# Optimization experiments

Measured on AMD Instinct MI355X. Metric: run time of the kernel, lower is better.

Reference implementation:

```python
import math
import jax, jax.numpy as jnp
import numpy as np

EMB = 1024
NHEADS = 16
CTX = 2048
LN_EPS = 1e-5


def new_gelu(x):
    c = math.sqrt(2.0 / math.pi)
    return 0.5 * x * (1.0 + jnp.tanh(c * (x + 0.044715 * x * x * x)))


def layer_norm(x, g, b):
    mu = jnp.mean(x, axis=-1, keepdims=True)
    var = jnp.mean(jnp.square(x - mu), axis=-1, keepdims=True)
    return (x - mu) * jax.lax.rsqrt(var + LN_EPS) * g + b


def setup_inputs() -> dict:
    key = jax.random.key(0)
    ks = jax.random.split(key, 12)
    s = 0.02
    return {
        "x": jax.random.normal(ks[0], (2, 2048, EMB), dtype=jnp.float32),
        "ln1_g": jnp.ones((EMB,), jnp.float32),
        "ln1_b": jnp.zeros((EMB,), jnp.float32),
        "W_attn": jax.random.normal(ks[1], (EMB, 3 * EMB), jnp.float32) * s,
        "b_attn": jnp.zeros((3 * EMB,), jnp.float32),
        "W_attn_proj": jax.random.normal(ks[2], (EMB, EMB), jnp.float32) * s,
        "b_attn_proj": jnp.zeros((EMB,), jnp.float32),
        "ln2_g": jnp.ones((EMB,), jnp.float32),
        "ln2_b": jnp.zeros((EMB,), jnp.float32),
        "W_fc": jax.random.normal(ks[3], (EMB, 4 * EMB), jnp.float32) * s,
        "b_fc": jnp.zeros((4 * EMB,), jnp.float32),
        "W_mlp_proj": jax.random.normal(ks[4], (4 * EMB, EMB), jnp.float32) * s,
        "b_mlp_proj": jnp.zeros((EMB,), jnp.float32),
    }


def reference(x, ln1_g, ln1_b, W_attn, b_attn, W_attn_proj, b_attn_proj,
              ln2_g, ln2_b, W_fc, b_fc, W_mlp_proj, b_mlp_proj):
    B, S, E = x.shape
    hd = E // NHEADS

    # x = ln_1(x)
    x = layer_norm(x, ln1_g, ln1_b)

    # attention on normalized x
    qkv = x @ W_attn + b_attn                      # [B,S,3E]
    q, k, v = jnp.split(qkv, 3, axis=-1)
    q = q.reshape(B, S, NHEADS, hd).transpose(0, 2, 1, 3)  # [B,H,S,hd]
    k = k.reshape(B, S, NHEADS, hd).transpose(0, 2, 1, 3)
    v = v.reshape(B, S, NHEADS, hd).transpose(0, 2, 1, 3)

    attn = jnp.einsum("bhqd,bhkd->bhqk", q, k) * (1.0 / math.sqrt(hd))
    causal = jnp.tril(jnp.ones((S, S), dtype=bool))
    attn = jnp.where(causal[None, None], attn, -jnp.inf)
    attn = jax.nn.softmax(attn, axis=-1)
    out = jnp.einsum("bhqk,bhkd->bhqd", attn, v)   # [B,H,S,hd]
    out = out.transpose(0, 2, 1, 3).reshape(B, S, E)
    out = out @ W_attn_proj + b_attn_proj

    x = x + out

    # x = ln_2(x)
    x = layer_norm(x, ln2_g, ln2_b)

    # MLP on normalized x
    h = new_gelu(x @ W_fc + b_fc)
    h = h @ W_mlp_proj + b_mlp_proj
    return x + h
```

## Files before the change

kernel.cpp:

```cpp
#include <hip/hip_runtime.h>
#include <cstdint>

typedef __attribute__((ext_vector_type(8))) short bf16x8;
typedef __attribute__((ext_vector_type(4))) float f32x4;
typedef __attribute__((ext_vector_type(4))) unsigned short u16x4;
typedef unsigned short u16;

#define LOG2E 1.44269504088896340736f

__device__ __forceinline__ u16 f2bf(float f) {
  unsigned u = __builtin_bit_cast(unsigned, f);
  u += 0x7FFFu + ((u >> 16) & 1u);
  return (u16)(u >> 16);
}
__device__ __forceinline__ float bf2f(u16 h) {
  return __builtin_bit_cast(float, ((unsigned)h) << 16);
}

#define GLOAD_LDS16(g, l)                                                              \
  __builtin_amdgcn_global_load_lds((const __attribute__((address_space(1))) void*)(g), \
                                   (__attribute__((address_space(3))) void*)(l), 16, 0, 0)

__global__ __launch_bounds__(256) void k_transpose_bf16(
    const float* __restrict__ W, u16* __restrict__ Wt, int K, int N) {
  __shared__ float tile[32][33];
  const int tid = threadIdx.x;
  const int tx = tid & 31, ty = tid >> 5;
  const int n0 = blockIdx.x * 32, k0 = blockIdx.y * 32;
#pragma unroll
  for (int i = 0; i < 32; i += 8)
    tile[ty + i][tx] = W[(size_t)(k0 + ty + i) * N + n0 + tx];
  __syncthreads();
#pragma unroll
  for (int i = 0; i < 32; i += 8)
    Wt[(size_t)(n0 + ty + i) * K + k0 + tx] = f2bf(tile[tx][ty + i]);
}

__global__ __launch_bounds__(256) void k_layernorm_bf16(
    const float* __restrict__ x, const float* __restrict__ g,
    const float* __restrict__ b, u16* __restrict__ y) {
  const int row = blockIdx.x, tid = threadIdx.x;
  const float4 v = ((const float4*)(x + (size_t)row * 1024))[tid];
  float s = v.x + v.y + v.z + v.w;
#pragma unroll
  for (int m = 1; m < 64; m <<= 1) s += __shfl_xor(s, m);
  __shared__ float ps[8];
  if ((tid & 63) == 0) ps[tid >> 6] = s;
  __syncthreads();
  const float mean = (ps[0] + ps[1] + ps[2] + ps[3]) * (1.0f / 1024.0f);
  const float d0 = v.x - mean, d1 = v.y - mean, d2 = v.z - mean, d3 = v.w - mean;
  float s2 = d0 * d0 + d1 * d1 + d2 * d2 + d3 * d3;
#pragma unroll
  for (int m = 1; m < 64; m <<= 1) s2 += __shfl_xor(s2, m);
  if ((tid & 63) == 0) ps[4 + (tid >> 6)] = s2;
  __syncthreads();
  const float var = (ps[4] + ps[5] + ps[6] + ps[7]) * (1.0f / 1024.0f);
  const float rstd = rsqrtf(var + 1e-5f);
  const float4 gv = ((const float4*)g)[tid];
  const float4 bv = ((const float4*)b)[tid];
  u16x4 o;
  o[0] = f2bf(d0 * rstd * gv.x + bv.x);
  o[1] = f2bf(d1 * rstd * gv.y + bv.y);
  o[2] = f2bf(d2 * rstd * gv.z + bv.z);
  o[3] = f2bf(d3 * rstd * gv.w + bv.w);
  *(u16x4*)(y + (size_t)row * 1024 + tid * 4) = o;
}

__device__ __forceinline__ float gelu_f(float x) {
  const float u = 0.7978845608028654f * (x + 0.044715f * x * x * x);
  const float e = exp2f(u * 2.8853900817779268f);
  const float t = 1.0f - 2.0f / (e + 1.0f);
  return 0.5f * x * (1.0f + t);
}

template <int EPI>
__global__ __launch_bounds__(256, 2) void k_gemm_bt(
    const u16* __restrict__ A, const u16* __restrict__ Bt,
    const float* __restrict__ bias, const u16* __restrict__ resid,
    void* __restrict__ out, u16* __restrict__ vt, int M, int N, int K) {
  __shared__ u16 As[2][128 * 64];
  __shared__ u16 Bs[2][128 * 64];
  const int tid = threadIdx.x;
  const int rowBase = blockIdx.y * 128, colBase = blockIdx.x * 128;
  const int w = tid >> 6, l = tid & 63;
  const int wm = w >> 1, wn = w & 1;
  const int lrow = l & 15, lg = l >> 4;
  const int srow = tid >> 3, sslot = tid & 7;

  const f32x4 fz = {0.f, 0.f, 0.f, 0.f};
  f32x4 acc[4][4];
#pragma unroll
  for (int m = 0; m < 4; m++)
#pragma unroll
    for (int n = 0; n < 4; n++) acc[m][n] = fz;

  const int NT = K >> 6;
  auto STAGE = [&](int b, int kt) {
#pragma unroll
    for (int i = 0; i < 4; i++) {
      const int r = srow + 32 * i;
      const int gs = sslot ^ (r & 7);
      GLOAD_LDS16(A + (size_t)(rowBase + r) * K + kt * 64 + gs * 8,
                  (char*)As[b] + i * 4096 + tid * 16);
      GLOAD_LDS16(Bt + (size_t)(colBase + r) * K + kt * 64 + gs * 8,
                  (char*)Bs[b] + i * 4096 + tid * 16);
    }
  };

  STAGE(0, 0);
  for (int kt = 0; kt < NT; ++kt) {
    const int buf = kt & 1;
    if (kt + 1 < NT) {
      STAGE(buf ^ 1, kt + 1);
      asm volatile("s_waitcnt vmcnt(8)" ::: "memory");
    } else {
      asm volatile("s_waitcnt vmcnt(0)" ::: "memory");
    }
    __builtin_amdgcn_s_barrier();
    const char* Ab = (const char*)As[buf];
    const char* Bb = (const char*)Bs[buf];
#pragma unroll
    for (int kc = 0; kc < 2; kc++) {
      bf16x8 av[4], bv[4];
#pragma unroll
      for (int m = 0; m < 4; m++) {
        const int r = wm * 64 + m * 16 + lrow;
        const int sl = (kc * 4 + lg) ^ (r & 7);
        av[m] = *(const bf16x8*)(Ab + r * 128 + sl * 16);
      }
#pragma unroll
      for (int n = 0; n < 4; n++) {
        const int r = wn * 64 + n * 16 + lrow;
        const int sl = (kc * 4 + lg) ^ (r & 7);
        bv[n] = *(const bf16x8*)(Bb + r * 128 + sl * 16);
      }
#pragma unroll
      for (int m = 0; m < 4; m++)
#pragma unroll
        for (int n = 0; n < 4; n++)
          acc[m][n] = __builtin_amdgcn_mfma_f32_16x16x32_bf16(av[m], bv[n], acc[m][n], 0, 0, 0);
    }
    __builtin_amdgcn_s_barrier();
  }
#pragma unroll
  for (int n = 0; n < 4; n++) {
    const int col = colBase + wn * 64 + n * 16 + lrow;
    const float bval = bias[col];
#pragma unroll
    for (int m = 0; m < 4; m++) {
      const int row0 = rowBase + wm * 64 + m * 16 + lg * 4;
#pragma unroll
      for (int r = 0; r < 4; r++) {
        const size_t idx = (size_t)(row0 + r) * N + col;
        float v = acc[m][n][r] + bval;
        if (EPI == 0) {
          ((u16*)out)[idx] = f2bf(v);
        } else if (EPI == 2) {
          ((u16*)out)[idx] = f2bf(gelu_f(v));
        } else {
          v += bf2f(resid[idx]);
          ((float*)out)[idx] = v;
        }
      }
    }
  }
}

template <int EPI>
__global__ __launch_bounds__(512, 1) void k_gemm8(
    const u16* __restrict__ A, const u16* __restrict__ Bt,
    const float* __restrict__ bias, void* __restrict__ out,
    u16* __restrict__ vt, int M, int N, int K, int nbx) {
  extern __shared__ char sm[];
  char* smA = sm;
  char* smB = sm + 65536;
  const int tid = threadIdx.x;
  const int q8 = gridDim.x >> 3;
  const int wg = (blockIdx.x & 7) * q8 + (blockIdx.x >> 3);
  const int bx = wg % nbx, by = wg / nbx;
  const int rowBase = by * 256, colBase = bx * 256;
  const int w = tid >> 6, l = tid & 63;
  const int wm = w >> 2, wn = w & 3;
  const int lrow = l & 15, lg = l >> 4;

  const int sArow = tid >> 3;
  const int gsA = (tid & 7) ^ (sArow & 7);
  const int sBrow = tid >> 2;
  const int gsB = (tid & 3) ^ ((tid >> 3) & 3);
  const u16* Ag = A + (size_t)(rowBase + sArow) * K + gsA * 8;
  const u16* Bg = Bt + (size_t)(colBase + sBrow) * K + gsB * 8;

#define STAGE_A8(buf, half, kt)                                                         \
  do {                                                                                  \
    GLOAD_LDS16(Ag + ((size_t)(half)*128) * K + (kt)*64,                                \
                smA + (buf)*32768 + (half)*16384 + tid * 16);                           \
    GLOAD_LDS16(Ag + ((size_t)(half)*128 + 64) * K + (kt)*64,                           \
                smA + (buf)*32768 + (half)*16384 + 8192 + tid * 16);                    \
  } while (0)
#define STAGE_B8(buf, ksl, kt)                                                          \
  do {                                                                                  \
    GLOAD_LDS16(Bg + (size_t)(kt)*64 + (ksl)*32,                                        \
                smB + (buf)*32768 + (ksl)*16384 + tid * 16);                            \
    GLOAD_LDS16(Bg + (size_t)128 * K + (kt)*64 + (ksl)*32,                              \
                smB + (buf)*32768 + (ksl)*16384 + 8192 + tid * 16);                     \
  } while (0)

  const int physB = lg ^ ((lrow >> 1) & 3);

  const f32x4 fz = {0.f, 0.f, 0.f, 0.f};
  f32x4 acc[8][4];
#pragma unroll
  for (int m = 0; m < 8; m++)
#pragma unroll
    for (int n = 0; n < 4; n++) acc[m][n] = fz;

  const int NT = K >> 6;
  STAGE_A8(0, 0, 0);
  STAGE_A8(0, 1, 0);
  STAGE_B8(0, 0, 0);
  STAGE_B8(0, 1, 0);

  for (int kt = 0; kt < NT; ++kt) {
    const int buf = kt & 1, nb = buf ^ 1, nxt = kt + 1;
    const bool pf = nxt < NT;
    const char* Ab = smA + buf * 32768 + wm * 16384;
    const char* Bb = smB + buf * 32768;

    asm volatile("s_waitcnt vmcnt(2)" ::: "memory");
    __builtin_amdgcn_s_barrier();

    bf16x8 a0[4], a1[4], b0[4], b1[4];
#pragma unroll
    for (int i = 0; i < 4; i++) {
      const int r = i * 16 + lrow;
      a0[i] = *(const bf16x8*)(Ab + r * 128 + ((lg) ^ (r & 7)) * 16);
    }
#pragma unroll
    for (int i = 0; i < 4; i++) {
      const int r = wn * 64 + i * 16 + lrow;
      b0[i] = *(const bf16x8*)(Bb + r * 64 + physB * 16);
    }
    if (pf) {
      STAGE_A8(nb, 0, nxt);
      STAGE_A8(nb, 1, nxt);
    }
    __builtin_amdgcn_s_setprio(1);
#pragma unroll
    for (int m = 0; m < 4; m++)
#pragma unroll
      for (int n = 0; n < 4; n++)
        acc[m][n] = __builtin_amdgcn_mfma_f32_16x16x32_bf16(a0[m], b0[n], acc[m][n], 0, 0, 0);
    __builtin_amdgcn_s_setprio(0);
#pragma unroll
    for (int i = 0; i < 4; i++) {
      const int r = (4 + i) * 16 + lrow;
      a1[i] = *(const bf16x8*)(Ab + r * 128 + ((lg) ^ (r & 7)) * 16);
    }
    if (pf) {
      STAGE_B8(nb, 0, nxt);
      STAGE_B8(nb, 1, nxt);
    }
    __builtin_amdgcn_s_setprio(1);
#pragma unroll
    for (int m = 0; m < 4; m++)
#pragma unroll
      for (int n = 0; n < 4; n++)
        acc[4 + m][n] = __builtin_amdgcn_mfma_f32_16x16x32_bf16(a1[m], b0[n], acc[4 + m][n], 0, 0, 0);
    __builtin_amdgcn_s_setprio(0);

    if (pf) {
      asm volatile("s_waitcnt vmcnt(8)" ::: "memory");
    } else {
      asm volatile("s_waitcnt vmcnt(0)" ::: "memory");
    }
    __builtin_amdgcn_s_barrier();

#pragma unroll
    for (int i = 0; i < 4; i++) {
      const int r = i * 16 + lrow;
      a0[i] = *(const bf16x8*)(Ab + r * 128 + ((4 + lg) ^ (r & 7)) * 16);
    }
#pragma unroll
    for (int i = 0; i < 4; i++) {
      const int r = wn * 64 + i * 16 + lrow;
      b1[i] = *(const bf16x8*)(Bb + 16384 + r * 64 + physB * 16);
    }
    __builtin_amdgcn_s_setprio(1);
#pragma unroll
    for (int m = 0; m < 4; m++)
#pragma unroll
      for (int n = 0; n < 4; n++)
        acc[m][n] = __builtin_amdgcn_mfma_f32_16x16x32_bf16(a0[m], b1[n], acc[m][n], 0, 0, 0);
    __builtin_amdgcn_s_setprio(0);
#pragma unroll
    for (int i = 0; i < 4; i++) {
      const int r = (4 + i) * 16 + lrow;
      a1[i] = *(const bf16x8*)(Ab + r * 128 + ((4 + lg) ^ (r & 7)) * 16);
    }
    __builtin_amdgcn_s_setprio(1);
#pragma unroll
    for (int m = 0; m < 4; m++)
#pragma unroll
      for (int n = 0; n < 4; n++)
        acc[4 + m][n] = __builtin_amdgcn_mfma_f32_16x16x32_bf16(a1[m], b1[n], acc[4 + m][n], 0, 0, 0);
    __builtin_amdgcn_s_setprio(0);
  }

#pragma unroll
  for (int n = 0; n < 4; n++) {
    const int col = colBase + wn * 64 + n * 16 + lrow;
    const float bval = bias[col];
#pragma unroll
    for (int m = 0; m < 8; m++) {
      const int row0 = rowBase + wm * 128 + m * 16 + lg * 4;
      if (EPI == 3 && col >= 2048) {
        const int c2 = col - 2048;
        const int hh = c2 >> 6, dd = c2 & 63;
        const int bat = row0 >> 11, tok0 = row0 & 2047;
        u16x4 pk;
#pragma unroll
        for (int r = 0; r < 4; r++) pk[r] = f2bf(acc[m][n][r] + bval);
        *(u16x4*)(vt + ((size_t)(bat * 16 + hh) * 64 + dd) * 2048 + tok0) = pk;
      } else if (EPI == 3) {
#pragma unroll
        for (int r = 0; r < 4; r++)
          ((u16*)out)[(size_t)(row0 + r) * 2048 + col] = f2bf(acc[m][n][r] + bval);
      } else if (EPI == 2) {
#pragma unroll
        for (int r = 0; r < 4; r++)
          ((u16*)out)[(size_t)(row0 + r) * N + col] = f2bf(gelu_f(acc[m][n][r] + bval));
      } else {
#pragma unroll
        for (int r = 0; r < 4; r++)
          ((u16*)out)[(size_t)(row0 + r) * N + col] = f2bf(acc[m][n][r] + bval);
      }
    }
  }
#undef STAGE_A8
#undef STAGE_B8
}

__global__ __launch_bounds__(256, 2) void k_attention(
    const u16* __restrict__ qk, const u16* __restrict__ VT, u16* __restrict__ out) {
  const int S = 2048, E2 = 2048;
  const int bid = blockIdx.x;
  const int pid = bid >> 5;
  const int bh = bid & 31;
  const int bat = bh >> 4, h = bh & 15;
  const u16* base = qk + (size_t)bat * S * E2;
  const u16* kbase = base + 1024 + h * 64;
  const u16* vbase = VT + (size_t)bh * 64 * S;
  const int tid = threadIdx.x, w = tid >> 6, l = tid & 63;
  const int lrow = l & 15, lg = l >> 4;
  __shared__ u16 Ks[2][64 * 64];
  __shared__ u16 Vs[2][64 * 64];
  __shared__ u16 Pl[4][16 * 64];
  u16* Plw = Pl[w];
  const int srow = tid >> 3, sslot = tid & 7;
  const int gs = sslot ^ (srow & 7);
  const float sc = 0.125f * LOG2E;
  const f32x4 fz = {0.f, 0.f, 0.f, 0.f};

  auto STAGE = [&](int bufi, int kb) {
#pragma unroll
    for (int round = 0; round < 2; round++) {
      const int r = srow + 32 * round;
      GLOAD_LDS16(kbase + (size_t)(kb + r) * E2 + gs * 8, (char*)Ks[bufi] + round * 4096 + tid * 16);
      GLOAD_LDS16(vbase + (size_t)r * S + kb + gs * 8, (char*)Vs[bufi] + round * 4096 + tid * 16);
    }
  };

  for (int pass = 0; pass < 2; ++pass) {
    const int qt = pass ? (31 - pid) : pid;
    const int qrow0 = qt * 64 + w * 16;
    const int nkt = qt + 1;

    bf16x8 qfrag[2];
#pragma unroll
    for (int kc = 0; kc < 2; kc++)
      qfrag[kc] = *(const bf16x8*)(base + (size_t)(qrow0 + lrow) * E2 + h * 64 + kc * 32 + lg * 8);

    f32x4 o[4];
    float mrow[4], lsum[4];
#pragma unroll
    for (int r = 0; r < 4; r++) { mrow[r] = -1e30f; lsum[r] = 0.f; }
#pragma unroll
    for (int df = 0; df < 4; df++) o[df] = fz;

    STAGE(0, 0);
    __syncthreads();

    for (int kt = 0; kt < nkt; kt++) {
      const int cur = kt & 1;
      const int kb = kt * 64;
      if (kt + 1 < nkt) STAGE(cur ^ 1, kb + 64);
      const u16* Kc = Ks[cur];
      const u16* Vc = Vs[cur];

      f32x4 sv[4];
#pragma unroll
      for (int kf = 0; kf < 4; kf++) sv[kf] = fz;
#pragma unroll
      for (int kc = 0; kc < 2; kc++) {
        bf16x8 kfr[4];
#pragma unroll
        for (int kf = 0; kf < 4; kf++) {
          const int rk = kf * 16 + lrow;
          kfr[kf] = *(const bf16x8*)(Kc + rk * 64 + ((kc * 4 + lg) ^ (rk & 7)) * 8);
        }
#pragma unroll
        for (int kf = 0; kf < 4; kf++)
          sv[kf] = __builtin_amdgcn_mfma_f32_16x16x32_bf16(qfrag[kc], kfr[kf], sv[kf], 0, 0, 0);
      }
#pragma unroll
      for (int kf = 0; kf < 4; kf++)
#pragma unroll
        for (int r = 0; r < 4; r++) sv[kf][r] *= sc;
      if (kt == nkt - 1) {
#pragma unroll
        for (int kf = 0; kf < 4; kf++) {
          const int kg = kb + kf * 16 + lrow;
#pragma unroll
          for (int r = 0; r < 4; r++) {
            const int qg = qrow0 + lg * 4 + r;
            if (kg > qg) sv[kf][r] = -1e30f;
          }
        }
      }
#pragma unroll
      for (int r = 0; r < 4; r++) {
        float mx = fmaxf(fmaxf(sv[0][r], sv[1][r]), fmaxf(sv[2][r], sv[3][r]));
#pragma unroll
        for (int msk = 1; msk < 16; msk <<= 1) mx = fmaxf(mx, __shfl_xor(mx, msk));
        const float mnew = fmaxf(mrow[r], mx);
        const float corr = exp2f(mrow[r] - mnew);
        mrow[r] = mnew;
        lsum[r] *= corr;
#pragma unroll
        for (int df = 0; df < 4; df++) o[df][r] *= corr;
        float rsv = 0.f;
#pragma unroll
        for (int kf = 0; kf < 4; kf++) {
          const float p = exp2f(sv[kf][r] - mnew);
          sv[kf][r] = p;
          rsv += p;
        }
#pragma unroll
        for (int msk = 1; msk < 16; msk <<= 1) rsv += __shfl_xor(rsv, msk);
        lsum[r] += rsv;
      }
#pragma unroll
      for (int kf = 0; kf < 4; kf++)
#pragma unroll
        for (int r = 0; r < 4; r++) {
          const int q = lg * 4 + r;
          *(u16*)((char*)Plw + q * 128 + ((kf * 32 + lrow * 2) ^ ((q & 7) << 4))) = f2bf(sv[kf][r]);
        }
#pragma unroll
      for (int kc = 0; kc < 2; kc++) {
        const bf16x8 pa =
            *(const bf16x8*)((const char*)Plw + lrow * 128 + (((kc * 4 + lg) ^ (lrow & 7)) << 4));
        bf16x8 vb[4];
#pragma unroll
        for (int df = 0; df < 4; df++) {
          const int rd = df * 16 + lrow;
          vb[df] = *(const bf16x8*)(Vc + rd * 64 + ((kc * 4 + lg) ^ (rd & 7)) * 8);
        }
#pragma unroll
        for (int df = 0; df < 4; df++)
          o[df] = __builtin_amdgcn_mfma_f32_16x16x32_bf16(pa, vb[df], o[df], 0, 0, 0);
      }
      __syncthreads();
    }
#pragma unroll
    for (int r = 0; r < 4; r++) {
      const float inv = 1.0f / lsum[r];
      const int qg = qrow0 + lg * 4 + r;
#pragma unroll
      for (int df = 0; df < 4; df++) {
        const int col = h * 64 + df * 16 + lrow;
        out[(size_t)(bat * S + qg) * 1024 + col] = f2bf(o[df][r] * inv);
      }
    }
  }
}

extern "C" void kernel_launch(void* const* d_in, const int* in_sizes, int n_in,
                              void* d_out, int out_size, void* d_ws, size_t ws_size,
                              hipStream_t stream) {
  (void)in_sizes; (void)n_in; (void)out_size; (void)ws_size;
  const float* x      = (const float*)d_in[0];
  const float* ln1_g  = (const float*)d_in[1];
  const float* ln1_b  = (const float*)d_in[2];
  const float* W_attn = (const float*)d_in[3];
  const float* b_attn = (const float*)d_in[4];
  const float* W_proj = (const float*)d_in[5];
  const float* b_proj = (const float*)d_in[6];
  const float* ln2_g  = (const float*)d_in[7];
  const float* ln2_b  = (const float*)d_in[8];
  const float* W_fc   = (const float*)d_in[9];
  const float* b_fc   = (const float*)d_in[10];
  const float* W_mlp  = (const float*)d_in[11];
  const float* b_mlp  = (const float*)d_in[12];

  const int M = 4096;
  char* ws = (char*)d_ws;
  size_t off = 0;
  auto alloc = [&](size_t bytes) {
    void* p = ws + off;
    off += (bytes + 255) & ~(size_t)255;
    return p;
  };
  u16* WattnT = (u16*)alloc((size_t)3072 * 1024 * 2);
  u16* WprojT = (u16*)alloc((size_t)1024 * 1024 * 2);
  u16* WfcT   = (u16*)alloc((size_t)4096 * 1024 * 2);
  u16* WmlpT  = (u16*)alloc((size_t)1024 * 4096 * 2);
  u16* x1     = (u16*)alloc((size_t)M * 1024 * 2);
  u16* qkb    = (u16*)alloc((size_t)M * 2048 * 2);
  u16* VT     = (u16*)alloc((size_t)32 * 64 * 2048 * 2);
  u16* attno  = (u16*)alloc((size_t)M * 1024 * 2);
  float* x2   = (float*)alloc((size_t)M * 1024 * 4);
  u16* x3     = (u16*)alloc((size_t)M * 1024 * 2);
  u16* hbuf   = (u16*)alloc((size_t)M * 4096 * 2);

  static bool attr_done = false;
  if (!attr_done) {
    hipFuncSetAttribute((const void*)k_gemm8<3>, hipFuncAttributeMaxDynamicSharedMemorySize, 131072);
    hipFuncSetAttribute((const void*)k_gemm8<2>, hipFuncAttributeMaxDynamicSharedMemorySize, 131072);
    attr_done = true;
  }

  const dim3 blk(256);
  k_transpose_bf16<<<dim3(3072 / 32, 1024 / 32), blk, 0, stream>>>(W_attn, WattnT, 1024, 3072);
  k_transpose_bf16<<<dim3(1024 / 32, 1024 / 32), blk, 0, stream>>>(W_proj, WprojT, 1024, 1024);
  k_transpose_bf16<<<dim3(4096 / 32, 1024 / 32), blk, 0, stream>>>(W_fc, WfcT, 1024, 4096);
  k_transpose_bf16<<<dim3(1024 / 32, 4096 / 32), blk, 0, stream>>>(W_mlp, WmlpT, 4096, 1024);

  k_layernorm_bf16<<<M, blk, 0, stream>>>(x, ln1_g, ln1_b, x1);
  k_gemm8<3><<<dim3((3072 / 256) * (M / 256)), dim3(512), 131072, stream>>>(
      x1, WattnT, b_attn, qkb, VT, M, 3072, 1024, 3072 / 256);
  k_attention<<<dim3(512), blk, 0, stream>>>(qkb, VT, attno);
  k_gemm_bt<1><<<dim3(1024 / 128, M / 128), blk, 0, stream>>>(attno, WprojT, b_proj, x1, x2, nullptr, M, 1024, 1024);
  k_layernorm_bf16<<<M, blk, 0, stream>>>(x2, ln2_g, ln2_b, x3);
  k_gemm8<2><<<dim3((4096 / 256) * (M / 256)), dim3(512), 131072, stream>>>(
      x3, WfcT, b_fc, hbuf, nullptr, M, 4096, 1024, 4096 / 256);
  k_gemm_bt<1><<<dim3(1024 / 128, M / 128), blk, 0, stream>>>(hbuf, WmlpT, b_mlp, x3, d_out, nullptr, M, 1024, 4096);
}
```

Baseline: 273.5 us.

## Restructure GEMM main loop into four barrier-separated LDS-load/MFMA phases

Reorganizes the bf16 GEMM k-loop into four phases. Each phase loads an A/B fragment from LDS, issues one quarter of the next tile's global-to-LDS prefetch, then runs a barrier, an lgkmcnt wait and a sched_barrier before its MFMA block. Register fragment arrays shrink from four to two, and the vmcnt wait points move so the loop-top wait happens at the end of the previous iteration. The goal is to interleave memory traffic more evenly with MFMA work across waves and lower register pressure, at the cost of several extra workgroup barriers per k-tile.

```diff
diff --git a/kernel.cpp b/kernel.cpp
--- a/kernel.cpp
+++ b/kernel.cpp
@@ -219,57 +219,57 @@
   STAGE_A8(0, 1, 0);
   STAGE_B8(0, 0, 0);
   STAGE_B8(0, 1, 0);
+  asm volatile("s_waitcnt vmcnt(2)" ::: "memory");
+  __builtin_amdgcn_s_barrier();
 
   for (int kt = 0; kt < NT; ++kt) {
     const int buf = kt & 1, nb = buf ^ 1, nxt = kt + 1;
     const bool pf = nxt < NT;
     const char* Ab = smA + buf * 32768 + wm * 16384;
     const char* Bb = smB + buf * 32768;
-
-    asm volatile("s_waitcnt vmcnt(2)" ::: "memory");
-    __builtin_amdgcn_s_barrier();
-
-    bf16x8 a0[4], a1[4], b0[4], b1[4];
+    bf16x8 a[4], b[4];
+
 #pragma unroll
     for (int i = 0; i < 4; i++) {
       const int r = i * 16 + lrow;
-      a0[i] = *(const bf16x8*)(Ab + r * 128 + ((lg) ^ (r & 7)) * 16);
-    }
-#pragma unroll
-    for (int i = 0; i < 4; i++) {
-      const int r = wn * 64 + i * 16 + lrow;
-      b0[i] = *(const bf16x8*)(Bb + r * 64 + physB * 16);
-    }
-    if (pf) {
-      STAGE_A8(nb, 0, nxt);
-      STAGE_A8(nb, 1, nxt);
-    }
+      a[i] = *(const bf16x8*)(Ab + r * 128 + ((lg) ^ (r & 7)) * 16);
+    }
+#pragma unroll
+    for (int n = 0; n < 4; n++) {
+      const int r = wn * 64 + n * 16 + lrow;
+      b[n] = *(const bf16x8*)(Bb + r * 64 + physB * 16);
+    }
+    if (pf) STAGE_A8(nb, 0, nxt);
+    __builtin_amdgcn_s_barrier();
+    asm volatile("s_waitcnt lgkmcnt(0)" ::: "memory");
+    __builtin_amdgcn_sched_barrier(0);
     __builtin_amdgcn_s_setprio(1);
 #pragma unroll
     for (int m = 0; m < 4; m++)
 #pragma unroll
       for (int n = 0; n < 4; n++)
-        acc[m][n] = __builtin_amdgcn_mfma_f32_16x16x32_bf16(a0[m], b0[n], acc[m][n], 0, 0, 0);
+        acc[m][n] = __builtin_amdgcn_mfma_f32_16x16x32_bf16(a[m], b[n], acc[m][n], 0, 0, 0);
     __builtin_amdgcn_s_setprio(0);
+    __builtin_amdgcn_s_barrier();
+
 #pragma unroll
     for (int i = 0; i < 4; i++) {
       const int r = (4 + i) * 16 + lrow;
-      a1[i] = *(const bf16x8*)(Ab + r * 128 + ((lg) ^ (r & 7)) * 16);
-    }
+      a[i] = *(const bf16x8*)(Ab + r * 128 + ((lg) ^ (r & 7)) * 16);
+    }
+    if (pf) STAGE_A8(nb, 1, nxt);
+    __builtin_amdgcn_s_barrier();
+    asm volatile("s_waitcnt lgkmcnt(0)" ::: "memory");
+    __builtin_amdgcn_sched_barrier(0);
+    __builtin_amdgcn_s_setprio(1);
+#pragma unroll
+    for (int m = 0; m < 4; m++)
+#pragma unroll
+      for (int n = 0; n < 4; n++)
+        acc[4 + m][n] = __builtin_amdgcn_mfma_f32_16x16x32_bf16(a[m], b[n], acc[4 + m][n], 0, 0, 0);
+    __builtin_amdgcn_s_setprio(0);
     if (pf) {
-      STAGE_B8(nb, 0, nxt);
-      STAGE_B8(nb, 1, nxt);
-    }
-    __builtin_amdgcn_s_setprio(1);
-#pragma unroll
-    for (int m = 0; m < 4; m++)
-#pragma unroll
-      for (int n = 0; n < 4; n++)
-        acc[4 + m][n] = __builtin_amdgcn_mfma_f32_16x16x32_bf16(a1[m], b0[n], acc[4 + m][n], 0, 0, 0);
-    __builtin_amdgcn_s_setprio(0);
-
-    if (pf) {
-      asm volatile("s_waitcnt vmcnt(8)" ::: "memory");
+      asm volatile("s_waitcnt vmcnt(4)" ::: "memory");
     } else {
       asm volatile("s_waitcnt vmcnt(0)" ::: "memory");
     }
@@ -278,32 +278,44 @@
 #pragma unroll
     for (int i = 0; i < 4; i++) {
       const int r = i * 16 + lrow;
-      a0[i] = *(const bf16x8*)(Ab + r * 128 + ((4 + lg) ^ (r & 7)) * 16);
-    }
-#pragma unroll
-    for (int i = 0; i < 4; i++) {
-      const int r = wn * 64 + i * 16 + lrow;
-      b1[i] = *(const bf16x8*)(Bb + 16384 + r * 64 + physB * 16);
-    }
+      a[i] = *(const bf16x8*)(Ab + r * 128 + ((4 + lg) ^ (r & 7)) * 16);
+    }
+#pragma unroll
+    for (int n = 0; n < 4; n++) {
+      const int r = wn * 64 + n * 16 + lrow;
+      b[n] = *(const bf16x8*)(Bb + 16384 + r * 64 + physB * 16);
+    }
+    if (pf) STAGE_B8(nb, 0, nxt);
+    __builtin_amdgcn_s_barrier();
+    asm volatile("s_waitcnt lgkmcnt(0)" ::: "memory");
+    __builtin_amdgcn_sched_barrier(0);
     __builtin_amdgcn_s_setprio(1);
 #pragma unroll
     for (int m = 0; m < 4; m++)
 #pragma unroll
       for (int n = 0; n < 4; n++)
-        acc[m][n] = __builtin_amdgcn_mfma_f32_16x16x32_bf16(a0[m], b1[n], acc[m][n], 0, 0, 0);
+        acc[m][n] = __builtin_amdgcn_mfma_f32_16x16x32_bf16(a[m], b[n], acc[m][n], 0, 0, 0);
     __builtin_amdgcn_s_setprio(0);
+    __builtin_amdgcn_s_barrier();
+
 #pragma unroll
     for (int i = 0; i < 4; i++) {
       const int r = (4 + i) * 16 + lrow;
-      a1[i] = *(const bf16x8*)(Ab + r * 128 + ((4 + lg) ^ (r & 7)) * 16);
-    }
+      a[i] = *(const bf16x8*)(Ab + r * 128 + ((4 + lg) ^ (r & 7)) * 16);
+    }
+    if (pf) STAGE_B8(nb, 1, nxt);
+    __builtin_amdgcn_s_barrier();
+    asm volatile("s_waitcnt lgkmcnt(0)" ::: "memory");
+    __builtin_amdgcn_sched_barrier(0);
     __builtin_amdgcn_s_setprio(1);
 #pragma unroll
     for (int m = 0; m < 4; m++)
 #pragma unroll
       for (int n = 0; n < 4; n++)
-        acc[4 + m][n] = __builtin_amdgcn_mfma_f32_16x16x32_bf16(a1[m], b1[n], acc[4 + m][n], 0, 0, 0);
+        acc[4 + m][n] = __builtin_amdgcn_mfma_f32_16x16x32_bf16(a[m], b[n], acc[4 + m][n], 0, 0, 0);
     __builtin_amdgcn_s_setprio(0);
+    asm volatile("s_waitcnt vmcnt(2)" ::: "memory");
+    __builtin_amdgcn_s_barrier();
   }
 
 #pragma unroll
```

Result: no change. 277.0 us (+1.3%).
